# Optimization experiments

Measured on AMD Instinct MI355X. Metric: run time of the kernel, lower is better.

Reference implementation:

```python
import jax, jax.numpy as jnp
import numpy as np

N_NODES = 50000
N_EDGES = 400000
IN_DIM = 64
HID = 128
HEADS = 4
NEG_SLOPE = 0.2


def gat_conv(x, src, dst, W, a_src, a_dst, b, heads, out_ch, concat):
    N = x.shape[0]
    h = (x @ W).reshape(N, heads, out_ch)                 # [N,H,C]
    alpha_s = jnp.einsum('nhc,hc->nh', h, a_src)          # [N,H]
    alpha_d = jnp.einsum('nhc,hc->nh', h, a_dst)
    e = jax.nn.leaky_relu(alpha_s[src] + alpha_d[dst], NEG_SLOPE)  # [E,H]
    m = jax.ops.segment_max(e, dst, num_segments=N)
    m = jnp.where(jnp.isfinite(m), m, 0.0)
    ex = jnp.exp(e - m[dst])
    s = jax.ops.segment_sum(ex, dst, num_segments=N)
    alpha = ex / s[dst]                                   # segment softmax over incoming edges
    out = jax.ops.segment_sum(h[src] * alpha[:, :, None], dst, num_segments=N)  # [N,H,C]
    out = out.reshape(N, heads * out_ch) if concat else out.mean(axis=1)
    return out + b


def setup_inputs() -> dict:
    key = jax.random.key(0)
    ks = jax.random.split(key, 20)
    g = lambda i, shape, sc: (jax.random.normal(ks[i], shape, jnp.float32) * sc)
    x = g(0, (N_NODES, IN_DIM), 1.0)
    edge_index = jax.random.randint(ks[1], (2, N_EDGES), 0, N_NODES, dtype=jnp.int32)
    d = {
        'x': x, 'edge_index': edge_index,
        'W1': g(2, (IN_DIM, HEADS * HID), 0.1), 'a_src1': g(3, (HEADS, HID), 0.1), 'a_dst1': g(4, (HEADS, HID), 0.1), 'b1': jnp.zeros((HEADS * HID,), jnp.float32),
        'W2': g(5, (HEADS * HID, HEADS * HID), 0.05), 'a_src2': g(6, (HEADS, HID), 0.1), 'a_dst2': g(7, (HEADS, HID), 0.1), 'b2': jnp.zeros((HEADS * HID,), jnp.float32),
        'W3': g(8, (HEADS * HID, HID), 0.05), 'a_src3': g(9, (1, HID), 0.1), 'a_dst3': g(10, (1, HID), 0.1), 'b3': jnp.zeros((HID,), jnp.float32),
        'fc1_w': g(11, (HID, HID // 2), 0.1), 'fc1_b': jnp.zeros((HID // 2,), jnp.float32),
        'fc2_w': g(12, (HID // 2, 1), 0.1), 'fc2_b': jnp.zeros((1,), jnp.float32),
    }
    return d


def reference(x, edge_index, W1, a_src1, a_dst1, b1, W2, a_src2, a_dst2, b2, W3, a_src3, a_dst3, b3, fc1_w, fc1_b, fc2_w, fc2_b):
    N = x.shape[0]
    loop = jnp.arange(N, dtype=edge_index.dtype)
    src = jnp.concatenate([edge_index[0], loop])  # PyG GATConv adds self-loops by default
    dst = jnp.concatenate([edge_index[1], loop])
    h = jax.nn.elu(gat_conv(x, src, dst, W1, a_src1, a_dst1, b1, HEADS, HID, True))
    h = jax.nn.elu(gat_conv(h, src, dst, W2, a_src2, a_dst2, b2, HEADS, HID, True))
    h = jax.nn.elu(gat_conv(h, src, dst, W3, a_src3, a_dst3, b3, 1, HID, False))
    h = jax.nn.relu(h @ fc1_w + fc1_b)
    return jax.nn.sigmoid(h @ fc2_w + fc2_b)  # [N, 1]
```

## Files before the change

### kernel.cpp

```cpp
#include <hip/hip_runtime.h>
#include <math.h>

typedef __attribute__((ext_vector_type(8))) short short8;
typedef __attribute__((ext_vector_type(4))) float f32x4;
typedef unsigned short u16;
typedef unsigned int u32;

__device__ inline u16 f2b(float f) {
  u32 u = __float_as_uint(f);
  return (u16)((u + 0x7FFFu + ((u >> 16) & 1u)) >> 16);
}
__device__ inline float b2f(u16 b) { return __uint_as_float((u32)b << 16); }
__device__ inline float lrelu(float v) { return v > 0.f ? v : 0.2f * v; }

__device__ inline void gld_lds16(const void* g, void* l) {
  __builtin_amdgcn_global_load_lds((const __attribute__((address_space(1))) void*)g,
                                   (__attribute__((address_space(3))) void*)l, 16, 0, 0);
}

__global__ void fused_prep(const float* __restrict__ x, u16* __restrict__ xb, int NX,
                           const float* __restrict__ W1, u16* __restrict__ Wt1,
                           const float* __restrict__ W2, u16* __restrict__ Wt2,
                           const float* __restrict__ W3, u16* __restrict__ Wt3,
                           const int* __restrict__ ei, int E0, int ET,
                           int* __restrict__ deg) {
  int i = blockIdx.x * blockDim.x + threadIdx.x;
  if (i < NX) {
    xb[i] = f2b(x[i]);
    return;
  }
  i -= NX;
  if (i < 64 * 512) {
    int k = i / 512, n = i % 512;
    Wt1[n * 64 + k] = f2b(W1[i]);
    return;
  }
  i -= 64 * 512;
  if (i < 512 * 512) {
    int k = i / 512, n = i % 512;
    Wt2[n * 512 + k] = f2b(W2[i]);
    return;
  }
  i -= 512 * 512;
  if (i < 512 * 128) {
    int k = i / 128, n = i % 128;
    Wt3[n * 512 + k] = f2b(W3[i]);
    return;
  }
  i -= 512 * 128;
  if (i < ET) {
    int d = (i < E0) ? ei[E0 + i] : (i - E0);
    atomicAdd(&deg[d], 1);
  }
}

__global__ __launch_bounds__(256) void gemm_bf16_gat(
    const u16* __restrict__ A, const u16* __restrict__ Bt, u16* __restrict__ Hb,
    const float* __restrict__ a_src, const float* __restrict__ a_dst,
    float* __restrict__ aS, float* __restrict__ aD, int M, int HC, int K, int Hh,
    int gy, int nStrips) {
  int mIdx, nIdx;
  if (nStrips == 4) {
    int l = blockIdx.x;
    int xcd = l & 7, k = l >> 3;
    nIdx = k & 3;
    mIdx = xcd + 8 * (k >> 2);
    if (mIdx >= gy) return;
  } else {
    mIdx = blockIdx.x;
    nIdx = 0;
  }
  __shared__ u16 As[128 * 32];
  __shared__ u16 Bs[128 * 32];
  __shared__ float sRed[2][2][128];
  const int tid = threadIdx.x;
  const int w = tid >> 6, lane = tid & 63;
  const int wm = w >> 1, wn = w & 1;
  const int q = lane >> 4, l15 = lane & 15;
  const int nBase = nIdx * 128;
  const int mBase = mIdx * 128;
  const int h = nBase >> 7;
  const int srow = lane >> 2;
  const int skc = (lane & 3) * 8;

  f32x4 acc[4][4];
#pragma unroll
  for (int i = 0; i < 4; ++i)
#pragma unroll
    for (int j = 0; j < 4; ++j) acc[i][j] = (f32x4){0.f, 0.f, 0.f, 0.f};

  for (int k0 = 0; k0 < K; k0 += 32) {
#pragma unroll
    for (int r = 0; r < 2; ++r) {
      int lrow = w * 32 + r * 16 + srow;
      int ga = mBase + lrow;
      if (ga >= M) ga = M - 1;
      gld_lds16(A + (size_t)ga * K + k0 + skc, &As[(w * 32 + r * 16) * 32]);
      int gb = nBase + lrow;
      gld_lds16(Bt + (size_t)gb * K + k0 + skc, &Bs[(w * 32 + r * 16) * 32]);
    }
    __syncthreads();
    short8 af[4], bf[4];
#pragma unroll
    for (int i = 0; i < 4; ++i)
      af[i] = *(const short8*)&As[(wm * 64 + i * 16 + l15) * 32 + q * 8];
#pragma unroll
    for (int j = 0; j < 4; ++j)
      bf[j] = *(const short8*)&Bs[(wn * 64 + j * 16 + l15) * 32 + q * 8];
#pragma unroll
    for (int i = 0; i < 4; ++i)
#pragma unroll
      for (int j = 0; j < 4; ++j)
        acc[i][j] = __builtin_amdgcn_mfma_f32_16x16x32_bf16(af[i], bf[j], acc[i][j], 0, 0, 0);
    __syncthreads();
  }

  float asv[4], adv[4];
#pragma unroll
  for (int j = 0; j < 4; ++j) {
    int cw = wn * 64 + j * 16 + l15;
    asv[j] = a_src[h * 128 + cw];
    adv[j] = a_dst[h * 128 + cw];
  }
#pragma unroll
  for (int mi = 0; mi < 4; ++mi) {
#pragma unroll
    for (int r = 0; r < 4; ++r) {
      int row = mBase + wm * 64 + mi * 16 + q * 4 + r;
      float s = 0.f, d = 0.f;
#pragma unroll
      for (int j = 0; j < 4; ++j) {
        float v = acc[mi][j][r];
        s = fmaf(v, asv[j], s);
        d = fmaf(v, adv[j], d);
        if (row < M) Hb[(size_t)row * HC + nBase + wn * 64 + j * 16 + l15] = f2b(v);
      }
#pragma unroll
      for (int o = 8; o; o >>= 1) {
        s += __shfl_xor(s, o);
        d += __shfl_xor(d, o);
      }
      if (l15 == 0) {
        int lr = wm * 64 + mi * 16 + q * 4 + r;
        sRed[0][wn][lr] = s;
        sRed[1][wn][lr] = d;
      }
    }
  }
  __syncthreads();
  if (tid < 128) {
    int row = mBase + tid;
    if (row < M) {
      aS[(size_t)row * Hh + h] = sRed[0][0][tid] + sRed[0][1][tid];
      aD[(size_t)row * Hh + h] = sRed[1][0][tid] + sRed[1][1][tid];
    }
  }
}

__global__ __launch_bounds__(256) void scan_chunk(const int* __restrict__ deg,
                                                  int* __restrict__ incl,
                                                  int* __restrict__ bsums, int N) {
  __shared__ int sdata[256];
  const int t = threadIdx.x;
  const int base = blockIdx.x * 2048;
  int v[8];
  int sum = 0;
#pragma unroll
  for (int i = 0; i < 8; ++i) {
    int idx = base + t * 8 + i;
    v[i] = (idx < N) ? deg[idx] : 0;
    sum += v[i];
  }
  sdata[t] = sum;
  __syncthreads();
  for (int off = 1; off < 256; off <<= 1) {
    int x = (t >= off) ? sdata[t - off] : 0;
    __syncthreads();
    sdata[t] += x;
    __syncthreads();
  }
  int run = (t > 0) ? sdata[t - 1] : 0;
#pragma unroll
  for (int i = 0; i < 8; ++i) {
    int idx = base + t * 8 + i;
    run += v[i];
    if (idx < N) incl[idx] = run;
  }
  if (t == 255) bsums[blockIdx.x] = sdata[255];
}

__global__ void scan_final(const int* __restrict__ incl, const int* __restrict__ bsums,
                           int* __restrict__ rowptr, int N, int nb) {
  int i = blockIdx.x * blockDim.x + threadIdx.x;
  if (i >= N) return;
  int chunk = i >> 11;
  int pre = 0;
  for (int j = 0; j < chunk; ++j) pre += bsums[j];
  rowptr[i + 1] = incl[i] + pre;
  if (i == 0) rowptr[0] = 0;
}

__global__ void csr_fill(const int* __restrict__ ei, int E0, int ET,
                         const int* __restrict__ rowptr, int* __restrict__ cnt,
                         int* __restrict__ csr_src) {
  int e = blockIdx.x * blockDim.x + threadIdx.x;
  if (e >= ET) return;
  int s, d;
  if (e < E0) { s = ei[e]; d = ei[E0 + e]; }
  else        { s = e - E0; d = e - E0; }
  int pos = atomicAdd(&cnt[d], 1);
  csr_src[rowptr[d] + pos] = s;
}

#define ACC8(pv, wgt)                                             \
  acc[0] = fmaf(wgt, b2f((u16)(pv.x & 0xffff)), acc[0]);          \
  acc[1] = fmaf(wgt, b2f((u16)(pv.x >> 16)), acc[1]);             \
  acc[2] = fmaf(wgt, b2f((u16)(pv.y & 0xffff)), acc[2]);          \
  acc[3] = fmaf(wgt, b2f((u16)(pv.y >> 16)), acc[3]);             \
  acc[4] = fmaf(wgt, b2f((u16)(pv.z & 0xffff)), acc[4]);          \
  acc[5] = fmaf(wgt, b2f((u16)(pv.z >> 16)), acc[5]);             \
  acc[6] = fmaf(wgt, b2f((u16)(pv.w & 0xffff)), acc[6]);          \
  acc[7] = fmaf(wgt, b2f((u16)(pv.w >> 16)), acc[7]);

__global__ __launch_bounds__(256) void gat_fused_agg(
    const int* __restrict__ rowptr, const int* __restrict__ csr_src,
    const u16* __restrict__ Hb, const float* __restrict__ aSb,
    const float* __restrict__ aDb, const float* __restrict__ bias,
    u16* __restrict__ outB, float* __restrict__ outF, int N) {
  const int wid = (int)((blockIdx.x * (blockDim.x >> 6)) + (threadIdx.x >> 6));
  const int lane = threadIdx.x & 63;
  if (wid >= N) return;
  const int beg = rowptr[wid];
  const int deg = rowptr[wid + 1] - beg;

  const int h = lane >> 4;
  const int e16 = lane & 15;
  const int c0 = lane * 8;
  const int hbase = lane & 48;
  const float adh = aDb[(size_t)wid * 4 + h];
  float bv[8];
  *(float4*)&bv[0] = *(const float4*)&bias[c0];
  *(float4*)&bv[4] = *(const float4*)&bias[c0 + 4];
  float m = -1e30f, ssum = 0.f;
  float acc[8] = {};
  for (int c = 0; c < deg; c += 16) {
    const int ce = min(16, deg - c);
    int srcv = 0;
    float l = -1e30f;
    if (e16 < ce) {
      srcv = csr_src[beg + c + e16];
      l = lrelu(aSb[(size_t)srcv * 4 + h] + adh);
    }
    float cm = l;
#pragma unroll
    for (int o = 8; o; o >>= 1) cm = fmaxf(cm, __shfl_xor(cm, o));
    float pexp, cs;
    if (c == 0) {
      m = cm;
      pexp = expf(l - m);
      cs = pexp;
#pragma unroll
      for (int o = 8; o; o >>= 1) cs += __shfl_xor(cs, o);
      ssum = cs;
    } else {
      float newm = fmaxf(m, cm);
      float r = expf(m - newm);
      m = newm;
      pexp = expf(l - m);
      cs = pexp;
#pragma unroll
      for (int o = 8; o; o >>= 1) cs += __shfl_xor(cs, o);
      ssum = ssum * r + cs;
#pragma unroll
      for (int i = 0; i < 8; ++i) acc[i] *= r;
    }
    int e = 0;
    for (; e + 4 <= ce; e += 4) {
      int se0 = __shfl(srcv, e + 0), se1 = __shfl(srcv, e + 1);
      int se2 = __shfl(srcv, e + 2), se3 = __shfl(srcv, e + 3);
      float w0 = __shfl(pexp, hbase | (e + 0)), w1 = __shfl(pexp, hbase | (e + 1));
      float w2 = __shfl(pexp, hbase | (e + 2)), w3 = __shfl(pexp, hbase | (e + 3));
      uint4 p0 = *(const uint4*)&Hb[(size_t)se0 * 512 + c0];
      uint4 p1 = *(const uint4*)&Hb[(size_t)se1 * 512 + c0];
      uint4 p2 = *(const uint4*)&Hb[(size_t)se2 * 512 + c0];
      uint4 p3 = *(const uint4*)&Hb[(size_t)se3 * 512 + c0];
      ACC8(p0, w0)
      ACC8(p1, w1)
      ACC8(p2, w2)
      ACC8(p3, w3)
    }
    for (; e < ce; ++e) {
      int se = __shfl(srcv, e);
      float wgt = __shfl(pexp, hbase | e);
      uint4 pv = *(const uint4*)&Hb[(size_t)se * 512 + c0];
      ACC8(pv, wgt)
    }
  }
  const float inv = 1.f / ssum;
  u16 packed[8];
#pragma unroll
  for (int i = 0; i < 8; ++i) {
    float v = fmaf(acc[i], inv, bv[i]);
    v = v > 0.f ? v : expm1f(v);
    acc[i] = v;
    packed[i] = f2b(v);
  }
  if (outB) *(uint4*)&outB[(size_t)wid * 512 + c0] = *(const uint4*)packed;
  if (outF) {
    *(float4*)&outF[(size_t)wid * 512 + c0] = make_float4(acc[0], acc[1], acc[2], acc[3]);
    *(float4*)&outF[(size_t)wid * 512 + c0 + 4] =
        make_float4(acc[4], acc[5], acc[6], acc[7]);
  }
}

__global__ __launch_bounds__(256) void gat_agg_h1(
    const int* __restrict__ rowptr, const int* __restrict__ csr_src,
    const u16* __restrict__ Hb, const float* __restrict__ aSb,
    const float* __restrict__ aDb, const float* __restrict__ bias,
    float* __restrict__ outF, int N) {
  const int wid = (int)((blockIdx.x * (blockDim.x >> 6)) + (threadIdx.x >> 6));
  const int lane = threadIdx.x & 63;
  if (wid >= N) return;
  const int beg = rowptr[wid];
  const int deg = rowptr[wid + 1] - beg;
  const int g = lane & 15;
  const int es = lane >> 4;
  const int c0 = g * 8;
  const float adh = aDb[wid];
  float m = -1e30f, ssum = 0.f;
  float acc[8] = {};
  for (int c = 0; c < deg; c += 64) {
    const int ce = min(64, deg - c);
    int srcv = 0;
    float l = -1e30f;
    if (lane < ce) {
      srcv = csr_src[beg + c + lane];
      l = lrelu(aSb[srcv] + adh);
    }
    float cm = l;
#pragma unroll
    for (int o = 32; o; o >>= 1) cm = fmaxf(cm, __shfl_xor(cm, o));
    float pexp, cs;
    if (c == 0) {
      m = cm;
      pexp = expf(l - m);
      cs = pexp;
#pragma unroll
      for (int o = 32; o; o >>= 1) cs += __shfl_xor(cs, o);
      ssum = cs;
    } else {
      float newm = fmaxf(m, cm);
      float r = expf(m - newm);
      m = newm;
      pexp = expf(l - m);
      cs = pexp;
#pragma unroll
      for (int o = 32; o; o >>= 1) cs += __shfl_xor(cs, o);
      ssum = ssum * r + cs;
#pragma unroll
      for (int i = 0; i < 8; ++i) acc[i] *= r;
    }
    for (int t = 0; t < ce; t += 4) {
      int idx = t + es;
      int se = __shfl(srcv, idx & 63);
      float wgt = __shfl(pexp, idx & 63);
      if (idx < ce) {
        uint4 pv = *(const uint4*)&Hb[(size_t)se * 128 + c0];
        ACC8(pv, wgt)
      }
    }
  }
#pragma unroll
  for (int i = 0; i < 8; ++i) {
    acc[i] += __shfl_xor(acc[i], 16);
    acc[i] += __shfl_xor(acc[i], 32);
  }
  if (lane < 16) {
    const float inv = 1.f / ssum;
    float o[8];
#pragma unroll
    for (int i = 0; i < 8; ++i) {
      float v = fmaf(acc[i], inv, bias[c0 + i]);
      o[i] = v > 0.f ? v : expm1f(v);
    }
    *(float4*)&outF[(size_t)wid * 128 + c0] = make_float4(o[0], o[1], o[2], o[3]);
    *(float4*)&outF[(size_t)wid * 128 + c0 + 4] = make_float4(o[4], o[5], o[6], o[7]);
  }
}

__global__ __launch_bounds__(256) void fc_head(const float* __restrict__ A,
                                               const float* __restrict__ B,
                                               const float* __restrict__ bias,
                                               const float* __restrict__ w2,
                                               const float* __restrict__ b2,
                                               float* __restrict__ out, int M) {
  __shared__ float As[16][64];
  __shared__ float Bs[16][64];
  __shared__ float sP[64][17];
  const int tid = threadIdx.x;
  const int tx = tid & 15, ty = tid >> 4;
  const int mBase = blockIdx.y * 64;
  const int aRow = tid >> 2;
  const int aK = (tid & 3) << 2;
  const int bC = tid & 63;
  const int bR0 = tid >> 6;
  const int K = 128, N = 64;
  float acc[4][4] = {};
  for (int k0 = 0; k0 < K; k0 += 16) {
    float4 av = make_float4(0.f, 0.f, 0.f, 0.f);
    int gr = mBase + aRow;
    if (gr < M) av = *(const float4*)&A[(size_t)gr * K + k0 + aK];
    As[aK + 0][aRow] = av.x;
    As[aK + 1][aRow] = av.y;
    As[aK + 2][aRow] = av.z;
    As[aK + 3][aRow] = av.w;
#pragma unroll
    for (int i = 0; i < 4; ++i) {
      int r = bR0 + i * 4;
      Bs[r][bC] = B[(size_t)(k0 + r) * N + bC];
    }
    __syncthreads();
#pragma unroll
    for (int k = 0; k < 16; ++k) {
      float4 a = *(const float4*)&As[k][ty * 4];
      float4 b = *(const float4*)&Bs[k][tx * 4];
      float ar[4] = {a.x, a.y, a.z, a.w};
      float br[4] = {b.x, b.y, b.z, b.w};
#pragma unroll
      for (int i = 0; i < 4; ++i)
#pragma unroll
        for (int j = 0; j < 4; ++j) acc[i][j] = fmaf(ar[i], br[j], acc[i][j]);
    }
    __syncthreads();
  }
  float4 bv = *(const float4*)&bias[tx * 4];
  float4 wv = *(const float4*)&w2[tx * 4];
#pragma unroll
  for (int i = 0; i < 4; ++i) {
    float p = 0.f;
    p = fmaf(fmaxf(acc[i][0] + bv.x, 0.f), wv.x, p);
    p = fmaf(fmaxf(acc[i][1] + bv.y, 0.f), wv.y, p);
    p = fmaf(fmaxf(acc[i][2] + bv.z, 0.f), wv.z, p);
    p = fmaf(fmaxf(acc[i][3] + bv.w, 0.f), wv.w, p);
    sP[ty * 4 + i][tx] = p;
  }
  __syncthreads();
  if (tid < 64) {
    int row = mBase + tid;
    if (row < M) {
      float s = 0.f;
#pragma unroll
      for (int t = 0; t < 16; ++t) s += sP[tid][t];
      out[row] = 1.f / (1.f + expf(-(s + b2[0])));
    }
  }
}

extern "C" void kernel_launch(void* const* d_in, const int* in_sizes, int n_in,
                              void* d_out, int out_size, void* d_ws, size_t ws_size,
                              hipStream_t stream) {
  const float* x    = (const float*)d_in[0];
  const int*   ei   = (const int*)d_in[1];
  const float* W1   = (const float*)d_in[2];
  const float* as1  = (const float*)d_in[3];
  const float* ad1  = (const float*)d_in[4];
  const float* b1   = (const float*)d_in[5];
  const float* W2   = (const float*)d_in[6];
  const float* as2  = (const float*)d_in[7];
  const float* ad2  = (const float*)d_in[8];
  const float* b2   = (const float*)d_in[9];
  const float* W3   = (const float*)d_in[10];
  const float* as3  = (const float*)d_in[11];
  const float* ad3  = (const float*)d_in[12];
  const float* b3   = (const float*)d_in[13];
  const float* fc1w = (const float*)d_in[14];
  const float* fc1b = (const float*)d_in[15];
  const float* fc2w = (const float*)d_in[16];
  const float* fc2b = (const float*)d_in[17];
  float* out = (float*)d_out;

  const int N  = in_sizes[0] / 64;
  const int E0 = in_sizes[1] / 2;
  const int ET = E0 + N;

  char* ws = (char*)d_ws;
  size_t off = 0;
  auto alloc = [&](size_t bytes) -> void* {
    void* p = ws + off;
    off += (bytes + 255) & ~(size_t)255;
    return p;
  };
  u16*   bufXb   = (u16*)alloc((size_t)N * 512 * 2);
  u16*   bufHb   = (u16*)alloc((size_t)N * 512 * 2);
  float* bufF    = (float*)alloc((size_t)N * 128 * 4);
  float* aS      = (float*)alloc((size_t)N * 4 * 4);
  float* aD      = (float*)alloc((size_t)N * 4 * 4);
  u16*   Wt1     = (u16*)alloc((size_t)512 * 64 * 2);
  u16*   Wt2     = (u16*)alloc((size_t)512 * 512 * 2);
  u16*   Wt3     = (u16*)alloc((size_t)128 * 512 * 2);
  int*   degcnt  = (int*)alloc((size_t)2 * N * 4);
  int*   deg     = degcnt;
  int*   cnt     = degcnt + N;
  int*   incl    = (int*)alloc((size_t)N * 4);
  int*   rowptr  = (int*)alloc((size_t)(N + 1) * 4);
  int*   bsums   = (int*)alloc(256 * 4);
  int*   csr_src = (int*)alloc((size_t)ET * 4);
  (void)ws_size; (void)n_in; (void)out_size;

  hipMemsetAsync(degcnt, 0, (size_t)2 * N * 4, stream);
  const int NX = N * 64;
  const int prepTotal = NX + 64 * 512 + 512 * 512 + 512 * 128 + ET;
  hipLaunchKernelGGL(fused_prep, dim3((prepTotal + 255) / 256), dim3(256), 0, stream, x,
                     bufXb, NX, W1, Wt1, W2, Wt2, W3, Wt3, ei, E0, ET, deg);

  int nb = (N + 2047) / 2048;
  hipLaunchKernelGGL(scan_chunk, dim3(nb), dim3(256), 0, stream, deg, incl, bsums, N);
  hipLaunchKernelGGL(scan_final, dim3((N + 255) / 256), dim3(256), 0, stream, incl, bsums,
                     rowptr, N, nb);
  int eb = (ET + 255) / 256;
  hipLaunchKernelGGL(csr_fill, dim3(eb), dim3(256), 0, stream, ei, E0, ET, rowptr, cnt,
                     csr_src);

  const int gy = (N + 127) / 128;
  const int grid4 = ((gy + 7) / 8) * 8 * 4;

  hipLaunchKernelGGL(gemm_bf16_gat, dim3(grid4), dim3(256), 0, stream, bufXb, Wt1, bufHb,
                     as1, ad1, aS, aD, N, 512, 64, 4, gy, 4);
  hipLaunchKernelGGL(gat_fused_agg, dim3((N + 3) / 4), dim3(256), 0, stream, rowptr,
                     csr_src, bufHb, aS, aD, b1, bufXb, nullptr, N);
  hipLaunchKernelGGL(gemm_bf16_gat, dim3(grid4), dim3(256), 0, stream, bufXb, Wt2, bufHb,
                     as2, ad2, aS, aD, N, 512, 512, 4, gy, 4);
  hipLaunchKernelGGL(gat_fused_agg, dim3((N + 3) / 4), dim3(256), 0, stream, rowptr,
                     csr_src, bufHb, aS, aD, b2, bufXb, nullptr, N);
  hipLaunchKernelGGL(gemm_bf16_gat, dim3(gy), dim3(256), 0, stream, bufXb, Wt3, bufHb,
                     as3, ad3, aS, aD, N, 128, 512, 1, gy, 1);
  hipLaunchKernelGGL(gat_agg_h1, dim3((N + 3) / 4), dim3(256), 0, stream, rowptr, csr_src,
                     bufHb, aS, aD, b3, bufF, N);

  hipLaunchKernelGGL(fc_head, dim3(1, (N + 63) / 64), dim3(256), 0, stream, bufF, fc1w,
                     fc1b, fc2w, fc2b, out, N);
}
```

Baseline: 457.4 us.

## Reorder layer-1 GAT to aggregate raw features before projecting

```diff
diff --git a/kernel.cpp b/kernel.cpp
--- a/kernel.cpp
+++ b/kernel.cpp
@@ -22,6 +22,8 @@
                            const float* __restrict__ W1, u16* __restrict__ Wt1,
                            const float* __restrict__ W2, u16* __restrict__ Wt2,
                            const float* __restrict__ W3, u16* __restrict__ Wt3,
+                           const float* __restrict__ as1, const float* __restrict__ ad1,
+                           float* __restrict__ wtil,
                            const int* __restrict__ ei, int E0, int ET,
                            int* __restrict__ deg) {
   int i = blockIdx.x * blockDim.x + threadIdx.x;
@@ -48,9 +50,233 @@
     return;
   }
   i -= 512 * 128;
+  if (i < 512) {
+    int v = i >> 8, rem = i & 255;
+    int h = rem >> 6, k = rem & 63;
+    const float* a = v ? ad1 : as1;
+    float s = 0.f;
+    for (int c = 0; c < 128; ++c) s = fmaf(W1[k * 512 + h * 128 + c], a[h * 128 + c], s);
+    wtil[i] = s;
+    return;
+  }
+  i -= 512;
   if (i < ET) {
     int d = (i < E0) ? ei[E0 + i] : (i - E0);
     atomicAdd(&deg[d], 1);
+  }
+}
+
+__global__ __launch_bounds__(256) void alpha_l1(const float* __restrict__ x,
+                                                const float* __restrict__ wtil,
+                                                float* __restrict__ aS,
+                                                float* __restrict__ aD, int N) {
+  __shared__ float sw[512];
+  const int tid = threadIdx.x;
+  sw[tid] = wtil[tid];
+  sw[tid + 256] = wtil[tid + 256];
+  __syncthreads();
+  int n = blockIdx.x * 256 + tid;
+  if (n >= N) return;
+  float s0 = 0.f, s1 = 0.f, s2 = 0.f, s3 = 0.f;
+  float d0 = 0.f, d1 = 0.f, d2 = 0.f, d3 = 0.f;
+  const float* xr = x + (size_t)n * 64;
+  for (int k = 0; k < 64; ++k) {
+    float xv = xr[k];
+    s0 = fmaf(xv, sw[k], s0);
+    s1 = fmaf(xv, sw[64 + k], s1);
+    s2 = fmaf(xv, sw[128 + k], s2);
+    s3 = fmaf(xv, sw[192 + k], s3);
+    d0 = fmaf(xv, sw[256 + k], d0);
+    d1 = fmaf(xv, sw[320 + k], d1);
+    d2 = fmaf(xv, sw[384 + k], d2);
+    d3 = fmaf(xv, sw[448 + k], d3);
+  }
+  *(float4*)&aS[(size_t)n * 4] = make_float4(s0, s1, s2, s3);
+  *(float4*)&aD[(size_t)n * 4] = make_float4(d0, d1, d2, d3);
+}
+
+__global__ __launch_bounds__(256) void gat_agg_l1(
+    const int* __restrict__ rowptr, const int* __restrict__ csr_src,
+    const u16* __restrict__ xb, const float* __restrict__ aSb,
+    const float* __restrict__ aDb, u16* __restrict__ xt, int N) {
+  const int wid = (int)((blockIdx.x * (blockDim.x >> 6)) + (threadIdx.x >> 6));
+  const int lane = threadIdx.x & 63;
+  if (wid >= N) return;
+  const int beg = rowptr[wid];
+  const int deg = rowptr[wid + 1] - beg;
+  const int h = lane >> 4;
+  const int e16 = lane & 15;
+  const int g = lane & 7;
+  const int es = lane >> 3;
+  const int c0 = g * 8;
+  const float adh = aDb[(size_t)wid * 4 + h];
+  float m = -1e30f, ssum = 0.f;
+  float a0[8] = {}, a1[8] = {}, a2[8] = {}, a3[8] = {};
+  for (int c = 0; c < deg; c += 16) {
+    const int ce = min(16, deg - c);
+    int srcv = 0;
+    float l = -1e30f;
+    if (e16 < ce) {
+      srcv = csr_src[beg + c + e16];
+      l = lrelu(aSb[(size_t)srcv * 4 + h] + adh);
+    }
+    float cm = l;
+#pragma unroll
+    for (int o = 8; o; o >>= 1) cm = fmaxf(cm, __shfl_xor(cm, o));
+    float pexp, cs;
+    if (c == 0) {
+      m = cm;
+      pexp = expf(l - m);
+      cs = pexp;
+#pragma unroll
+      for (int o = 8; o; o >>= 1) cs += __shfl_xor(cs, o);
+      ssum = cs;
+    } else {
+      float newm = fmaxf(m, cm);
+      float r = expf(m - newm);
+      m = newm;
+      pexp = expf(l - m);
+      cs = pexp;
+#pragma unroll
+      for (int o = 8; o; o >>= 1) cs += __shfl_xor(cs, o);
+      ssum = ssum * r + cs;
+#pragma unroll
+      for (int i = 0; i < 8; ++i) {
+        a0[i] *= r;
+        a1[i] *= r;
+        a2[i] *= r;
+        a3[i] *= r;
+      }
+    }
+    for (int t = 0; t < ce; t += 8) {
+      int idx = t + es;
+      int i15 = idx & 15;
+      int se = __shfl(srcv, i15);
+      float w0 = __shfl(pexp, i15);
+      float w1 = __shfl(pexp, 16 | i15);
+      float w2 = __shfl(pexp, 32 | i15);
+      float w3 = __shfl(pexp, 48 | i15);
+      if (idx < ce) {
+        uint4 pv = *(const uint4*)&xb[(size_t)se * 64 + c0];
+        u32 wd[4] = {pv.x, pv.y, pv.z, pv.w};
+#pragma unroll
+        for (int q2 = 0; q2 < 4; ++q2) {
+          float xv0 = b2f((u16)(wd[q2] & 0xffff));
+          float xv1 = b2f((u16)(wd[q2] >> 16));
+          int i0 = q2 * 2, i1 = q2 * 2 + 1;
+          a0[i0] = fmaf(w0, xv0, a0[i0]);
+          a0[i1] = fmaf(w0, xv1, a0[i1]);
+          a1[i0] = fmaf(w1, xv0, a1[i0]);
+          a1[i1] = fmaf(w1, xv1, a1[i1]);
+          a2[i0] = fmaf(w2, xv0, a2[i0]);
+          a2[i1] = fmaf(w2, xv1, a2[i1]);
+          a3[i0] = fmaf(w3, xv0, a3[i0]);
+          a3[i1] = fmaf(w3, xv1, a3[i1]);
+        }
+      }
+    }
+  }
+#pragma unroll
+  for (int i = 0; i < 8; ++i) {
+#pragma unroll
+    for (int o = 8; o <= 32; o <<= 1) {
+      a0[i] += __shfl_xor(a0[i], o);
+      a1[i] += __shfl_xor(a1[i], o);
+      a2[i] += __shfl_xor(a2[i], o);
+      a3[i] += __shfl_xor(a3[i], o);
+    }
+  }
+  float is0 = 1.f / __shfl(ssum, 0);
+  float is1 = 1.f / __shfl(ssum, 16);
+  float is2 = 1.f / __shfl(ssum, 32);
+  float is3 = 1.f / __shfl(ssum, 48);
+  if (lane < 8) {
+    u16 pk[8];
+#pragma unroll
+    for (int i = 0; i < 8; ++i) pk[i] = f2b(a0[i] * is0);
+    *(uint4*)&xt[(size_t)wid * 256 + c0] = *(const uint4*)pk;
+#pragma unroll
+    for (int i = 0; i < 8; ++i) pk[i] = f2b(a1[i] * is1);
+    *(uint4*)&xt[(size_t)wid * 256 + 64 + c0] = *(const uint4*)pk;
+#pragma unroll
+    for (int i = 0; i < 8; ++i) pk[i] = f2b(a2[i] * is2);
+    *(uint4*)&xt[(size_t)wid * 256 + 128 + c0] = *(const uint4*)pk;
+#pragma unroll
+    for (int i = 0; i < 8; ++i) pk[i] = f2b(a3[i] * is3);
+    *(uint4*)&xt[(size_t)wid * 256 + 192 + c0] = *(const uint4*)pk;
+  }
+}
+
+__global__ __launch_bounds__(256) void gemm_bf16_l1(
+    const u16* __restrict__ A, const u16* __restrict__ Bt,
+    const float* __restrict__ bias, u16* __restrict__ out, int M, int gy) {
+  int l = blockIdx.x;
+  int xcd = l & 7, kk = l >> 3;
+  int nIdx = kk & 3;
+  int mIdx = xcd + 8 * (kk >> 2);
+  if (mIdx >= gy) return;
+  __shared__ u16 As[128 * 32];
+  __shared__ u16 Bs[128 * 32];
+  const int tid = threadIdx.x;
+  const int w = tid >> 6, lane = tid & 63;
+  const int wm = w >> 1, wn = w & 1;
+  const int q = lane >> 4, l15 = lane & 15;
+  const int nBase = nIdx * 128;
+  const int mBase = mIdx * 128;
+  const int aOff = nIdx * 64;
+  const int srow = lane >> 2;
+  const int skc = (lane & 3) * 8;
+
+  f32x4 acc[4][4];
+#pragma unroll
+  for (int i = 0; i < 4; ++i)
+#pragma unroll
+    for (int j = 0; j < 4; ++j) acc[i][j] = (f32x4){0.f, 0.f, 0.f, 0.f};
+
+#pragma unroll
+  for (int k0 = 0; k0 < 64; k0 += 32) {
+#pragma unroll
+    for (int r = 0; r < 2; ++r) {
+      int lrow = w * 32 + r * 16 + srow;
+      int ga = mBase + lrow;
+      if (ga >= M) ga = M - 1;
+      gld_lds16(A + (size_t)ga * 256 + aOff + k0 + skc, &As[(w * 32 + r * 16) * 32]);
+      int gb = nBase + lrow;
+      gld_lds16(Bt + (size_t)gb * 64 + k0 + skc, &Bs[(w * 32 + r * 16) * 32]);
+    }
+    __syncthreads();
+    short8 af[4], bf[4];
+#pragma unroll
+    for (int i = 0; i < 4; ++i)
+      af[i] = *(const short8*)&As[(wm * 64 + i * 16 + l15) * 32 + q * 8];
+#pragma unroll
+    for (int j = 0; j < 4; ++j)
+      bf[j] = *(const short8*)&Bs[(wn * 64 + j * 16 + l15) * 32 + q * 8];
+#pragma unroll
+    for (int i = 0; i < 4; ++i)
+#pragma unroll
+      for (int j = 0; j < 4; ++j)
+        acc[i][j] = __builtin_amdgcn_mfma_f32_16x16x32_bf16(af[i], bf[j], acc[i][j], 0, 0, 0);
+    __syncthreads();
+  }
+
+  float bv[4];
+#pragma unroll
+  for (int j = 0; j < 4; ++j) bv[j] = bias[nBase + wn * 64 + j * 16 + l15];
+#pragma unroll
+  for (int mi = 0; mi < 4; ++mi) {
+#pragma unroll
+    for (int r = 0; r < 4; ++r) {
+      int row = mBase + wm * 64 + mi * 16 + q * 4 + r;
+      if (row < M) {
+#pragma unroll
+        for (int j = 0; j < 4; ++j) {
+          float v = acc[mi][j][r] + bv[j];
+          v = v > 0.f ? v : expm1f(v);
+          out[(size_t)row * 512 + nBase + wn * 64 + j * 16 + l15] = f2b(v);
+        }
+      }
+    }
   }
 }
 
@@ -492,12 +718,15 @@
   };
   u16*   bufXb   = (u16*)alloc((size_t)N * 512 * 2);
   u16*   bufHb   = (u16*)alloc((size_t)N * 512 * 2);
+  u16*   xb64    = (u16*)alloc((size_t)N * 64 * 2);
+  u16*   xt      = (u16*)alloc((size_t)N * 256 * 2);
   float* bufF    = (float*)alloc((size_t)N * 128 * 4);
   float* aS      = (float*)alloc((size_t)N * 4 * 4);
   float* aD      = (float*)alloc((size_t)N * 4 * 4);
   u16*   Wt1     = (u16*)alloc((size_t)512 * 64 * 2);
   u16*   Wt2     = (u16*)alloc((size_t)512 * 512 * 2);
   u16*   Wt3     = (u16*)alloc((size_t)128 * 512 * 2);
+  float* wtil    = (float*)alloc((size_t)512 * 4);
   int*   degcnt  = (int*)alloc((size_t)2 * N * 4);
   int*   deg     = degcnt;
   int*   cnt     = degcnt + N;
@@ -509,9 +738,9 @@
 
   hipMemsetAsync(degcnt, 0, (size_t)2 * N * 4, stream);
   const int NX = N * 64;
-  const int prepTotal = NX + 64 * 512 + 512 * 512 + 512 * 128 + ET;
+  const int prepTotal = NX + 64 * 512 + 512 * 512 + 512 * 128 + 512 + ET;
   hipLaunchKernelGGL(fused_prep, dim3((prepTotal + 255) / 256), dim3(256), 0, stream, x,
-                     bufXb, NX, W1, Wt1, W2, Wt2, W3, Wt3, ei, E0, ET, deg);
+                     xb64, NX, W1, Wt1, W2, Wt2, W3, Wt3, as1, ad1, wtil, ei, E0, ET, deg);
 
   int nb = (N + 2047) / 2048;
   hipLaunchKernelGGL(scan_chunk, dim3(nb), dim3(256), 0, stream, deg, incl, bsums, N);
@@ -524,10 +753,12 @@
   const int gy = (N + 127) / 128;
   const int grid4 = ((gy + 7) / 8) * 8 * 4;
 
-  hipLaunchKernelGGL(gemm_bf16_gat, dim3(grid4), dim3(256), 0, stream, bufXb, Wt1, bufHb,
-                     as1, ad1, aS, aD, N, 512, 64, 4, gy, 4);
-  hipLaunchKernelGGL(gat_fused_agg, dim3((N + 3) / 4), dim3(256), 0, stream, rowptr,
-                     csr_src, bufHb, aS, aD, b1, bufXb, nullptr, N);
+  hipLaunchKernelGGL(alpha_l1, dim3((N + 255) / 256), dim3(256), 0, stream, x, wtil, aS,
+                     aD, N);
+  hipLaunchKernelGGL(gat_agg_l1, dim3((N + 3) / 4), dim3(256), 0, stream, rowptr, csr_src,
+                     xb64, aS, aD, xt, N);
+  hipLaunchKernelGGL(gemm_bf16_l1, dim3(grid4), dim3(256), 0, stream, xt, Wt1, b1, bufXb,
+                     N, gy);
   hipLaunchKernelGGL(gemm_bf16_gat, dim3(grid4), dim3(256), 0, stream, bufXb, Wt2, bufHb,
                      as2, ad2, aS, aD, N, 512, 512, 4, gy, 4);
   hipLaunchKernelGGL(gat_fused_agg, dim3((N + 3) / 4), dim3(256), 0, stream, rowptr,
```

Result: no change. 463.2 us (+1.3%).
